# Kernel tuning notes

Measured on AMD Instinct MI355X. Metric: run time of the kernel, lower is better.

## Reference

```python
import jax, jax.numpy as jnp
import numpy as np
from jax import lax

D = 256; NH = 8; LYR = 2; G = 64; K = G * G; T = 4; EC = 32
B = 4; N = 512; CITY = 256; DFF = 4 * D

def _conv(x, w):
    return lax.conv_general_dilated(x, w, (1, 1), 'SAME', dimension_numbers=('NCHW', 'OIHW', 'NCHW'))

def _ln(x, w, b):
    m = x.mean(-1, keepdims=True)
    v = ((x - m) ** 2).mean(-1, keepdims=True)
    return (x - m) / jnp.sqrt(v + 1e-5) * w + b

def _mlp(x, w1, b1, w2, b2):
    return jax.nn.gelu(x @ w1 + b1) @ w2 + b2

def setup_inputs():
    key = jax.random.key(0)
    ks = iter(jax.random.split(key, 64))
    def nrm(shape, s=0.02):
        return jax.random.normal(next(ks), shape, jnp.float32) * s
    return {
        'meas_xy': jax.random.uniform(next(ks), (B, N, 2), jnp.float32),
        'meas_v': jax.random.normal(next(ks), (B, N), jnp.float32),
        'bs_xy': jax.random.uniform(next(ks), (B, 1, 2), jnp.float32),
        'task_id': jax.random.randint(next(ks), (B,), 0, T),
        'city': jax.random.uniform(next(ks), (B, CITY, CITY), jnp.float32),
        'mp_w1': nrm((3, D)), 'mp_b1': jnp.zeros((D,)), 'mp_w2': nrm((D, D)), 'mp_b2': jnp.zeros((D,)),
        'bp_w1': nrm((2, D)), 'bp_b1': jnp.zeros((D,)), 'bp_w2': nrm((D, D)), 'bp_b2': jnp.zeros((D,)),
        'env_w1': nrm((EC, 1, 3, 3)), 'env_b1': jnp.zeros((EC,)),
        'env_w2': nrm((EC, EC, 3, 3)), 'env_b2': jnp.zeros((EC,)),
        'env_w3': nrm((D, EC, 1, 1)), 'env_b3': jnp.zeros((D,)),
        'task_emb': nrm((T, D)), 'tp_w': nrm((D, D)), 'tp_b': jnp.zeros((D,)),
        'grid_pos': nrm((K, D)),
        'blk_dens_w': nrm((LYR, D)), 'blk_dens_b': jnp.zeros((LYR, D)),
        'blk_ln1_w': jnp.ones((LYR, D)), 'blk_ln1_b': jnp.zeros((LYR, D)),
        'blk_wq': nrm((LYR, D, D)), 'blk_bq': jnp.zeros((LYR, D)),
        'blk_wk': nrm((LYR, D, D)), 'blk_bk': jnp.zeros((LYR, D)),
        'blk_wv': nrm((LYR, D, D)), 'blk_bv': jnp.zeros((LYR, D)),
        'blk_wo': nrm((LYR, D, D)), 'blk_bo': jnp.zeros((LYR, D)),
        'blk_ln2_w': jnp.ones((LYR, D)), 'blk_ln2_b': jnp.zeros((LYR, D)),
        'blk_ff_w1': nrm((LYR, D, DFF)), 'blk_ff_b1': jnp.zeros((LYR, DFF)),
        'blk_ff_w2': nrm((LYR, DFF, D)), 'blk_ff_b2': jnp.zeros((LYR, D)),
        'tfp_w': nrm((T, D, D)), 'tfp_b': jnp.zeros((T, D)),
        'head_w': nrm((D, 1)), 'head_b': jnp.zeros((1,)),
    }

def reference(meas_xy, meas_v, bs_xy, task_id, city, mp_w1, mp_b1, mp_w2, mp_b2, bp_w1, bp_b1, bp_w2, bp_b2, env_w1, env_b1, env_w2, env_b2, env_w3, env_b3, task_emb, tp_w, tp_b, grid_pos, blk_dens_w, blk_dens_b, blk_ln1_w, blk_ln1_b, blk_wq, blk_bq, blk_wk, blk_bk, blk_wv, blk_bv, blk_wo, blk_bo, blk_ln2_w, blk_ln2_b, blk_ff_w1, blk_ff_b1, blk_ff_w2, blk_ff_b2, tfp_w, tfp_b, head_w, head_b):
    b = meas_xy.shape[0]
    dh = D // NH
    # normalized grid cell centers, [K,2] in (x,y) order
    c = (jnp.arange(G, dtype=jnp.float32) + 0.5) / G
    gy, gx = jnp.meshgrid(c, c, indexing='ij')
    grid_xy = jnp.stack([gx, gy], -1).reshape(K, 2)
    meas_tok = _mlp(jnp.concatenate([meas_xy, meas_v[..., None]], -1), mp_w1, mp_b1, mp_w2, mp_b2)
    bs_tok = _mlp(bs_xy, bp_w1, bp_b1, bp_w2, bp_b2)
    src = jnp.concatenate([meas_tok, bs_tok], 1)       # [B,Ns,D]
    src_xy = jnp.concatenate([meas_xy, bs_xy], 1)      # [B,Ns,2]
    # distance bias: [B,K,Ns]
    attn_bias = -jnp.linalg.norm(grid_xy[None, :, None, :] - src_xy[:, None, :, :], axis=-1)
    # gaussian measurement density: [B,K]
    diff = grid_xy[None, :, None, :] - meas_xy[:, None, :, :]
    dist2 = (diff * diff).sum(-1)
    sigma = 0.08
    density = jnp.exp(-dist2 / (2.0 * sigma * sigma)).mean(-1)
    # env branch: nearest-resize city to GxG, small CNN
    idx = jnp.floor(jnp.arange(G) * (city.shape[1] / G)).astype(jnp.int32)
    city_grid = city[:, idx][:, :, idx][:, None]       # [B,1,G,G]
    h = jax.nn.gelu(_conv(city_grid, env_w1) + env_b1[None, :, None, None])
    h = jax.nn.gelu(_conv(h, env_w2) + env_b2[None, :, None, None])
    env_map = _conv(h, env_w3) + env_b3[None, :, None, None]
    env_grid = env_map.transpose(0, 2, 3, 1).reshape(b, K, D)
    task_vec = (task_emb[task_id] @ tp_w + tp_b)[:, None, :]
    grid = grid_pos[None] + task_vec + env_grid
    inv_sqrt = jnp.float32(1.0 / np.sqrt(dh))
    for l in range(LYR):
        # density modulation injected into the grid latent
        g = grid + density[..., None] * blk_dens_w[l] + blk_dens_b[l]
        hn = _ln(g, blk_ln1_w[l], blk_ln1_b[l])
        q = (hn @ blk_wq[l] + blk_bq[l]).reshape(b, K, NH, dh)
        kk = (src @ blk_wk[l] + blk_bk[l]).reshape(b, -1, NH, dh)
        vv = (src @ blk_wv[l] + blk_bv[l]).reshape(b, -1, NH, dh)
        scores = jnp.einsum('bkhd,bnhd->bhkn', q, kk) * inv_sqrt + attn_bias[:, None]
        a = jax.nn.softmax(scores, -1)
        o = jnp.einsum('bhkn,bnhd->bkhd', a, vv).reshape(b, K, D) @ blk_wo[l] + blk_bo[l]
        g = g + o
        g = g + _mlp(_ln(g, blk_ln2_w[l], blk_ln2_b[l]), blk_ff_w1[l], blk_ff_b1[l], blk_ff_w2[l], blk_ff_b2[l])
        grid = g
    # per-sample task projection from the weight bank
    tf = jax.nn.gelu(jnp.einsum('bkd,bdh->bkh', grid, tfp_w[task_id]) + tfp_b[task_id][:, None, :])
    logits = (tf @ head_w + head_b)[..., 0].reshape(b, G, G)
    return logits
```

## Files before the change

### kernel.cpp

```cpp
#include <hip/hip_runtime.h>
#include <hip/hip_bf16.h>
#include <math.h>

#define D 256
#define NH 8
#define DH 32
#define LYR 2
#define G 64
#define KK 4096
#define T 4
#define EC 32
#define B 4
#define N 512
#define CITY 256
#define DFF 1024
#define NS 513
#define NSP 544
#define MSRC 2052
#define MSRCP 2176
#define ISQ 0.17677669529663687f
#define LOG2E 1.4426950408889634f

typedef short bf16x8 __attribute__((ext_vector_type(8)));
typedef float f32x4 __attribute__((ext_vector_type(4)));

__device__ __forceinline__ float gelu_f(float x) {
    const float c = 0.7978845608028654f;
    float x3 = x * x * x;
    return 0.5f * x * (1.f + tanhf(c * (x + 0.044715f * x3)));
}

__device__ __forceinline__ unsigned short f2bf(float f) {
    unsigned int u = __float_as_uint(f);
    unsigned int r = (u + 0x7FFFu + ((u >> 16) & 1u)) >> 16;
    return (unsigned short)r;
}

__device__ __forceinline__ float bf2f(unsigned short u) {
    return __uint_as_float((unsigned)u << 16);
}

__device__ __forceinline__ unsigned cvtpk(float a, float b) {
    unsigned r;
    asm("v_cvt_pk_bf16_f32 %0, %1, %2" : "=v"(r) : "v"(a), "v"(b));
    return r;
}

__device__ __forceinline__ void gl2lds16(const unsigned short* g, unsigned short* l) {
    __builtin_amdgcn_global_load_lds(
        (const __attribute__((address_space(1))) unsigned int*)g,
        (__attribute__((address_space(3))) unsigned int*)l, 16, 0, 0);
}

__global__ __launch_bounds__(256) void pre1_k(
    const float* __restrict__ wq, const float* __restrict__ wk,
    const float* __restrict__ wv, const float* __restrict__ wo,
    const float* __restrict__ ff1, const float* __restrict__ ff2,
    const float* __restrict__ tfp,
    const float* __restrict__ bk, const float* __restrict__ bv,
    unsigned short* __restrict__ wqT, unsigned short* __restrict__ kvT,
    unsigned short* __restrict__ woT, unsigned short* __restrict__ ff1T,
    unsigned short* __restrict__ ff2T, unsigned short* __restrict__ tfpT,
    float* __restrict__ kvbias,
    const float* __restrict__ meas_xy, const float* __restrict__ meas_v,
    const float* __restrict__ bs_xy,
    const float* __restrict__ mp_w1, const float* __restrict__ mp_b1,
    const float* __restrict__ mp_w2, const float* __restrict__ mp_b2,
    const float* __restrict__ bp_w1, const float* __restrict__ bp_b1,
    const float* __restrict__ bp_w2, const float* __restrict__ bp_b2,
    unsigned short* __restrict__ srcbf, float* __restrict__ src_xy,
    float* __restrict__ dens,
    const float* __restrict__ city, const float* __restrict__ env_w1,
    const float* __restrict__ env_b1, float* __restrict__ h1,
    const float* __restrict__ task_emb, const int* __restrict__ task_id,
    const float* __restrict__ tp_w, const float* __restrict__ tp_b,
    float* __restrict__ tvec,
    unsigned short* __restrict__ khd, unsigned short* __restrict__ vch)
{
    __shared__ float sh[1088];
    int bx = blockIdx.x;
    int tid = threadIdx.x;
    if (bx < 1792) {
        const float* src; unsigned short* dst;
        int Kd, Nn, nmat, rowOff = 0, t; size_t matStride;
        if (bx < 512) {
            int job = bx >> 7; t = bx & 127;
            Kd = 256; Nn = 256; nmat = 2;
            if (job == 0)      { src = wq; dst = wqT; matStride = 65536; }
            else if (job == 1) { src = wk; dst = kvT; matStride = 131072; }
            else if (job == 2) { src = wv; dst = kvT; matStride = 131072; rowOff = 256; }
            else               { src = wo; dst = woT; matStride = 65536; }
            if ((t & 63) == 0 && job == 1) kvbias[(t >> 6) * 512 + tid] = bk[(t >> 6) * 256 + tid];
            if ((t & 63) == 0 && job == 2) kvbias[(t >> 6) * 512 + 256 + tid] = bv[(t >> 6) * 256 + tid];
        } else if (bx < 1024) { t = bx - 512;  src = ff1; dst = ff1T; Kd = 256;  Nn = 1024; nmat = 2; matStride = 262144; }
        else if (bx < 1536)   { t = bx - 1024; src = ff2; dst = ff2T; Kd = 1024; Nn = 256;  nmat = 2; matStride = 262144; }
        else                  { t = bx - 1536; src = tfp; dst = tfpT; Kd = 256;  Nn = 256;  nmat = 4; matStride = 65536; }
        int tn = Nn / 32, perMat = tn * (Kd / 32);
        int mat = t / perMat;
        int rem = t - mat * perMat;
        int nb = (rem % tn) * 32, kb = (rem / tn) * 32;
        const float* s = src + (size_t)mat * Kd * Nn;
        unsigned short* d = dst + (size_t)mat * matStride;
        float (*tb)[33] = (float (*)[33])sh;
        int tx = tid & 31, ty = tid >> 5;
        #pragma unroll
        for (int i = 0; i < 4; i++)
            tb[ty + i * 8][tx] = s[(size_t)(kb + ty + i * 8) * Nn + nb + tx];
        __syncthreads();
        #pragma unroll
        for (int i = 0; i < 4; i++)
            d[(size_t)(rowOff + nb + ty + i * 8) * Kd + kb + tx] = f2bf(tb[tx][ty + i * 8]);
    } else if (bx < 3968) {
        int id = bx - 1792;
        int dd = tid;
        if (id >= B * N + B) {
            srcbf[(size_t)id * D + dd] = 0;
            return;
        }
        float* hid = sh;
        int row;
        const float *w1, *b1, *w2, *b2;
        float x0, x1, x2 = 0.f;
        int nin;
        if (id < B * N) {
            int b = id >> 9, n = id & 511;
            x0 = meas_xy[(b * N + n) * 2 + 0];
            x1 = meas_xy[(b * N + n) * 2 + 1];
            x2 = meas_v[b * N + n];
            w1 = mp_w1; b1 = mp_b1; w2 = mp_w2; b2 = mp_b2; nin = 3;
            row = b * NS + n;
        } else {
            int b = id - B * N;
            x0 = bs_xy[b * 2 + 0];
            x1 = bs_xy[b * 2 + 1];
            w1 = bp_w1; b1 = bp_b1; w2 = bp_w2; b2 = bp_b2; nin = 2;
            row = b * NS + N;
        }
        float h = x0 * w1[dd] + x1 * w1[D + dd] + b1[dd];
        if (nin == 3) h += x2 * w1[2 * D + dd];
        hid[dd] = gelu_f(h);
        __syncthreads();
        float o = b2[dd];
        for (int j = 0; j < D; j++) o += hid[j] * w2[j * D + dd];
        srcbf[(size_t)row * D + dd] = f2bf(o);
        if (dd == 0) { src_xy[row * 2 + 0] = x0; src_xy[row * 2 + 1] = x1; }
    } else if (bx < 4032) {
        int blk = bx - 3968;
        int b = blk >> 4, kc = blk & 15;
        int k = kc * 256 + tid;
        float* mx = sh; float* my = sh + 512;
        for (int i = tid; i < N; i += 256) {
            mx[i] = meas_xy[(b * N + i) * 2 + 0];
            my[i] = meas_xy[(b * N + i) * 2 + 1];
        }
        __syncthreads();
        float gx = ((k & 63) + 0.5f) / 64.f;
        float gy = ((k >> 6) + 0.5f) / 64.f;
        float s = 0.f;
        for (int n = 0; n < N; n++) {
            float dx = gx - mx[n], dy = gy - my[n];
            s += __expf(-(dx * dx + dy * dy) * 78.125f);
        }
        dens[b * KK + k] = s * (1.f / (float)N);
    } else if (bx < 6080) {
        int i = (bx - 4032) * 256 + tid;
        int x = i & 63, y = (i >> 6) & 63, c = (i >> 12) & 31, b = i >> 17;
        float s = env_b1[c];
        for (int ky = 0; ky < 3; ky++) {
            int yy = y + ky - 1;
            if (yy < 0 || yy >= G) continue;
            for (int kx = 0; kx < 3; kx++) {
                int xx = x + kx - 1;
                if (xx < 0 || xx >= G) continue;
                s += city[(b * CITY + yy * 4) * CITY + xx * 4] * env_w1[c * 9 + ky * 3 + kx];
            }
        }
        h1[i] = gelu_f(s);
    } else if (bx < 6084) {
        int b = bx - 6080;
        float* e = sh;
        e[tid] = task_emb[task_id[b] * D + tid];
        __syncthreads();
        float s = tp_b[tid];
        for (int j = 0; j < D; j++) s += e[j] * tp_w[j * D + tid];
        tvec[b * D + tid] = s;
    } else {
        int bh = bx - 6084;
        unsigned short* kp = khd + ((size_t)bh * 544 + 513) * 32;
        for (int i = tid; i < 992; i += 256) kp[i] = 0;
        unsigned short* vp = vch + ((size_t)bh * 17 + 16) * 1024;
        for (int i = tid; i < 1024; i += 256) vp[i] = 0;
    }
}

__global__ __launch_bounds__(256) void conv2_k(
    const float* __restrict__ h1, const float* __restrict__ w,
    const float* __restrict__ bias, float* __restrict__ h2) {
    int blk = blockIdx.x;
    int yt = blk & 15, cg = (blk >> 4) & 7, b = blk >> 7;
    int x = threadIdx.x & 63, y = yt * 4 + (threadIdx.x >> 6);
    int c0 = cg * 4;
    float flag[9];
    int off[9];
    #pragma unroll
    for (int ky = 0; ky < 3; ky++) {
        int yy = y + ky - 1;
        bool vy = (yy >= 0 && yy < G);
        int yc = min(max(yy, 0), G - 1);
        #pragma unroll
        for (int kx = 0; kx < 3; kx++) {
            int xx = x + kx - 1;
            bool vx = (xx >= 0 && xx < G);
            int xc = min(max(xx, 0), G - 1);
            flag[ky * 3 + kx] = (vy && vx) ? 1.f : 0.f;
            off[ky * 3 + kx] = yc * G + xc;
        }
    }
    const float* hp = h1 + ((size_t)(b * EC) << 12);
    float acc[4] = {bias[c0], bias[c0 + 1], bias[c0 + 2], bias[c0 + 3]};
    float v[9], nv[9];
    #pragma unroll
    for (int t = 0; t < 9; t++) v[t] = hp[off[t]] * flag[t];
    for (int ci = 0; ci < EC; ci++) {
        if (ci < EC - 1) {
            const float* hn = hp + ((size_t)(ci + 1) << 12);
            #pragma unroll
            for (int t = 0; t < 9; t++) nv[t] = hn[off[t]] * flag[t];
        }
        #pragma unroll
        for (int cc = 0; cc < 4; cc++) {
            const float* wp = w + ((size_t)(c0 + cc) * EC + ci) * 9;
            #pragma unroll
            for (int t = 0; t < 9; t++) acc[cc] += v[t] * wp[t];
        }
        #pragma unroll
        for (int t = 0; t < 9; t++) v[t] = nv[t];
    }
    size_t obase = (((size_t)(b * EC + c0)) << 12) + y * G + x;
    #pragma unroll
    for (int cc = 0; cc < 4; cc++)
        h2[obase + ((size_t)cc << 12)] = gelu_f(acc[cc]);
}

__global__ __launch_bounds__(256) void pre2_k(
    const float* __restrict__ h2, const float* __restrict__ w3,
    const float* __restrict__ b3, const float* __restrict__ grid_pos,
    const float* __restrict__ tvec, float* __restrict__ grid,
    const float* __restrict__ sxy, unsigned short* __restrict__ nd,
    float* __restrict__ out, const float* __restrict__ head_b)
{
    __shared__ float sh[1088];
    int bx = blockIdx.x;
    int tid = threadIdx.x;
    if (bx < 2048) {
        int b = bx >> 9, k0 = (bx & 511) * 8;
        float (*h2s)[8] = (float (*)[8])sh;
        h2s[tid >> 3][tid & 7] = h2[(((size_t)b * EC + (tid >> 3)) << 12) + k0 + (tid & 7)];
        float w3r[32];
        #pragma unroll
        for (int c4 = 0; c4 < 8; c4++) {
            float4 w4 = *(const float4*)(w3 + tid * 32 + c4 * 4);
            w3r[c4 * 4 + 0] = w4.x; w3r[c4 * 4 + 1] = w4.y;
            w3r[c4 * 4 + 2] = w4.z; w3r[c4 * 4 + 3] = w4.w;
        }
        float base = b3[tid] + tvec[b * D + tid];
        __syncthreads();
        #pragma unroll
        for (int j = 0; j < 8; j++) {
            float s = base + grid_pos[(size_t)(k0 + j) * D + tid];
            #pragma unroll
            for (int ci = 0; ci < 32; ci++) s += h2s[ci][j] * w3r[ci];
            grid[((size_t)b * KK + k0 + j) * D + tid] = s;
        }
    } else if (bx < 2304) {
        int q = bx - 2048;
        int b = q >> 6, qt = q & 63;
        float* sxs = sh; float* sys = sh + 544;
        for (int i = tid; i < 544; i += 256) {
            float x = 0.f, y = 0.f;
            if (i < NS) { x = sxy[(b * NS + i) * 2]; y = sxy[(b * NS + i) * 2 + 1]; }
            sxs[i] = x; sys[i] = y;
        }
        __syncthreads();
        unsigned short* base = nd + (size_t)q * 34816;
        for (int c = 0; c < 17; c++) {
            #pragma unroll
            for (int it = 0; it < 2; it++) {
                int lin = it * 256 + tid;
                int w16 = lin & 63, q4 = (lin >> 6) & 3, half = lin >> 8;
                int qidx = qt * 64 + w16;
                float gx = ((qidx & 63) + 0.5f) * (1.f / 64.f);
                float gy = ((qidx >> 6) + 0.5f) * (1.f / 64.f);
                unsigned short vs[4];
                #pragma unroll
                for (int r = 0; r < 4; r++) {
                    int tok = c * 32 + half * 16 + q4 * 4 + r;
                    float val;
                    if (tok < NS) {
                        float dx = gx - sxs[tok], dy = gy - sys[tok];
                        val = -sqrtf(dx * dx + dy * dy);
                    } else val = -1e4f;
                    vs[r] = f2bf(val * LOG2E);
                }
                ushort4 o; o.x = vs[0]; o.y = vs[1]; o.z = vs[2]; o.w = vs[3];
                *(ushort4*)(base + (size_t)c * 2048 + lin * 4) = o;
            }
        }
    } else {
        out[(bx - 2304) * 256 + tid] = head_b[0];
    }
}

template <int DENS>
__global__ __launch_bounds__(256) void dens_ln_k(
    float* __restrict__ grid, const float* __restrict__ dens,
    const float* __restrict__ dw, const float* __restrict__ db,
    const float* __restrict__ lw, const float* __restrict__ lb,
    unsigned short* __restrict__ y) {
    int row = blockIdx.x * 4 + (threadIdx.x >> 6);
    int lane = threadIdx.x & 63;
    float* gp = grid + (size_t)row * D + lane * 4;
    float4 v = *(float4*)gp;
    if (DENS) {
        float de = dens[row];
        float4 w4 = *(const float4*)(dw + lane * 4);
        float4 b4 = *(const float4*)(db + lane * 4);
        v.x += de * w4.x + b4.x; v.y += de * w4.y + b4.y;
        v.z += de * w4.z + b4.z; v.w += de * w4.w + b4.w;
        *(float4*)gp = v;
    }
    float s = v.x + v.y + v.z + v.w;
    #pragma unroll
    for (int o = 32; o > 0; o >>= 1) s += __shfl_xor(s, o);
    float mean = s * (1.f / D);
    float cx = v.x - mean, cy = v.y - mean, cz = v.z - mean, cw = v.w - mean;
    float q = cx * cx + cy * cy + cz * cz + cw * cw;
    #pragma unroll
    for (int o = 32; o > 0; o >>= 1) q += __shfl_xor(q, o);
    float inv = rsqrtf(q * (1.f / D) + 1e-5f);
    float4 lwv = *(const float4*)(lw + lane * 4);
    float4 lbv = *(const float4*)(lb + lane * 4);
    ushort4 o4;
    o4.x = f2bf(cx * inv * lwv.x + lbv.x);
    o4.y = f2bf(cy * inv * lwv.y + lbv.y);
    o4.z = f2bf(cz * inv * lwv.z + lbv.z);
    o4.w = f2bf(cw * inv * lwv.w + lbv.w);
    *(ushort4*)(y + (size_t)row * D + lane * 4) = o4;
}

template <int GELU, int ACCUM, int OBF, int TFPH, int STBF, int KVT = 0>
__device__ __forceinline__ void gemm_core(
    const unsigned short* __restrict__ A, const unsigned short* __restrict__ Wt,
    const float* __restrict__ bias, void* __restrict__ Cv,
    int M, int K, int Nn, int bn, int bm,
    const float* __restrict__ hw, unsigned short* __restrict__ Xb, float scale,
    unsigned short* As, unsigned short* Bs) {
    int tid = threadIdx.x;
    int wave = tid >> 6, lane = tid & 63;
    int q4 = lane >> 4, lr = lane & 15;
    int wn = wave * 16;
    int srow = tid >> 2, sk8 = (tid & 3) * 8;
    const unsigned short* Ap  = A  + (size_t)(bm + srow) * K + sk8;
    const unsigned short* Bp0 = Wt + (size_t)(bn + srow) * K + sk8;
    unsigned short* AsD = As + tid * 8;
    unsigned short* BsD = Bs + tid * 8;
    f32x4 acc[4] = {};

    gl2lds16(Ap,       AsD);
    gl2lds16(Ap + 32,  AsD + 2048);
    gl2lds16(Bp0,      BsD);
    gl2lds16(Bp0 + 32, BsD + 2048);

    int nk = K >> 6;
    for (int ki = 0; ki < nk; ki++) {
        __syncthreads();
        if (ki + 1 < nk) {
            int k0 = (ki + 1) << 6;
            int nb = ((ki + 1) & 1) * 4096;
            gl2lds16(Ap + k0,       AsD + nb);
            gl2lds16(Ap + k0 + 32,  AsD + nb + 2048);
            gl2lds16(Bp0 + k0,      BsD + nb);
            gl2lds16(Bp0 + k0 + 32, BsD + nb + 2048);
        }
        int cb = (ki & 1) * 4096;
        #pragma unroll
        for (int ks = 0; ks < 2; ks++) {
            bf16x8 af[4], bf;
            #pragma unroll
            for (int i = 0; i < 4; i++)
                af[i] = *(const bf16x8*)&As[cb + ks * 2048 + (i * 16 + lr) * 32 + q4 * 8];
            bf = *(const bf16x8*)&Bs[cb + ks * 2048 + (wn + lr) * 32 + q4 * 8];
            #pragma unroll
            for (int i = 0; i < 4; i++)
                acc[i] = __builtin_amdgcn_mfma_f32_16x16x32_bf16(af[i], bf, acc[i], 0, 0, 0);
        }
    }

    if (KVT) {
        int gc = bn + wn + lr;
        float bv = bias[gc];
        bool isV = gc >= 256;
        #pragma unroll
        for (int i = 0; i < 4; i++) {
            #pragma unroll
            for (int r = 0; r < 4; r++) {
                int gr = bm + i * 16 + q4 * 4 + r;
                if (gr < MSRC) {
                    float v = acc[i][r] + bv;
                    int bb = gr / NS;
                    int tok = gr - bb * NS;
                    if (!isV) {
                        int h = gc >> 5, dh = gc & 31;
                        ((unsigned short*)Cv)[(((size_t)(bb * 8 + h) * 544) + tok) * 32 + dh] = f2bf(v);
                    } else {
                        int gcv = gc - 256;
                        int h = gcv >> 5, dh = gcv & 31;
                        int c = tok >> 5, t32 = tok & 31;
                        Xb[((((size_t)(bb * 8 + h) * 17 + c) * 32 + dh)) * 32 + t32] = f2bf(v);
                    }
                }
            }
        }
        return;
    }

    if (TFPH) {
        int gc = bn + wn + lr;
        float bv = bias[gc];
        float hv = hw[gc];
        #pragma unroll
        for (int i = 0; i < 4; i++) {
            #pragma unroll
            for (int r = 0; r < 4; r++) {
                float s = gelu_f(acc[i][r] + bv) * hv;
                s += __shfl_xor(s, 1); s += __shfl_xor(s, 2);
                s += __shfl_xor(s, 4); s += __shfl_xor(s, 8);
                if (lr == 0)
                    atomicAdd((float*)Cv + (bm + i * 16 + q4 * 4 + r), s);
            }
        }
        return;
    }

    int gc = bn + wn + lr;
    float bv = bias[gc];
    #pragma unroll
    for (int i = 0; i < 4; i++) {
        #pragma unroll
        for (int r = 0; r < 4; r++) {
            int gr = bm + i * 16 + q4 * 4 + r;
            if (gr < M) {
                float v = (acc[i][r] + bv) * scale;
                if (GELU) v = gelu_f(v);
                size_t idx = (size_t)gr * Nn + gc;
                if (OBF) {
                    ((unsigned short*)Cv)[idx] = f2bf(v);
                } else if (ACCUM) {
                    float nv = ((float*)Cv)[idx] + v;
                    ((float*)Cv)[idx] = nv;
                    if (STBF) Xb[idx] = f2bf(nv);
                } else {
                    ((float*)Cv)[idx] = v;
                }
            }
        }
    }
}

template <int GELU, int ACCUM, int OBF, int TFPH, int STBF>
__global__ __launch_bounds__(256) void gemm_k(
    const unsigned short* __restrict__ A, const unsigned short* __restrict__ Wt0,
    const float* __restrict__ bias0, void* __restrict__ Cv,
    int M, int K, int Nn, const int* __restrict__ task_id,
    const float* __restrict__ hw, unsigned short* __restrict__ Xb) {
    __shared__ unsigned short As[8192];
    __shared__ unsigned short Bs[8192];
    const unsigned short* Wt = Wt0;
    const float* bias = bias0;
    int bm = blockIdx.y * 64;
    if (TFPH) { int t = task_id[bm >> 12]; Wt += (size_t)t * D * D; bias += t * D; }
    gemm_core<GELU, ACCUM, OBF, TFPH, STBF>(A, Wt, bias, Cv, M, K, Nn,
                                            blockIdx.x * 64, bm, hw, Xb, 1.f, As, Bs);
}

__global__ __launch_bounds__(256) void qkv_k(
    const unsigned short* __restrict__ xbf, const unsigned short* __restrict__ wqT,
    const float* __restrict__ bq, unsigned short* __restrict__ qbf,
    const unsigned short* __restrict__ srcbf, const unsigned short* __restrict__ kvT,
    const float* __restrict__ kvb, unsigned short* __restrict__ khd,
    unsigned short* __restrict__ vch) {
    __shared__ unsigned short As[8192];
    __shared__ unsigned short Bs[8192];
    if (blockIdx.x < 4) {
        gemm_core<0, 0, 1, 0, 0, 0>(xbf, wqT, bq, qbf, B * KK, D, D,
                                    blockIdx.x * 64, blockIdx.y * 64, nullptr, nullptr,
                                    ISQ * LOG2E, As, Bs);
    } else {
        if (blockIdx.y >= MSRCP / 64) return;
        gemm_core<0, 0, 1, 0, 0, 1>(srcbf, kvT, kvb, khd, MSRC, D, 512,
                                    (blockIdx.x - 4) * 64, blockIdx.y * 64, nullptr, vch, 1.f, As, Bs);
    }
}

__global__ __launch_bounds__(256) void attn_mfma(
    const unsigned short* __restrict__ qb,
    const unsigned short* __restrict__ khd,
    const unsigned short* __restrict__ vch,
    const unsigned short* __restrict__ ndL,
    unsigned short* __restrict__ out)
{
    int bid = blockIdx.x;
    int qt = bid & 63, h = (bid >> 6) & 7, b = bid >> 9;
    int tid = threadIdx.x, wave = tid >> 6, lane = tid & 63;
    int q4 = lane >> 4, lr = lane & 15;

    int kbase = qt * 64 + wave * 16;
    size_t qrow = (size_t)(b * KK + kbase + lr);
    bf16x8 qf = *(const bf16x8*)(qb + qrow * D + h * DH + q4 * 8);
    const unsigned short* kp0 = khd + ((size_t)(b * 8 + h) * 544) * 32 + lr * 32 + q4 * 8;
    const unsigned short* vb0 = vch + ((size_t)(b * 8 + h) * 17) * 1024 + lr * 32 + q4 * 8;
    const unsigned short* ndp = ndL + ((size_t)(b * 64 + qt)) * 34816 + q4 * 256 + (wave * 16 + lr) * 4;

    float ll0 = 0.f, ll1 = 0.f;
    f32x4 o0 = {0.f, 0.f, 0.f, 0.f}, o1 = {0.f, 0.f, 0.f, 0.f};
    int sA = ((lane >> 4) & 1) * 32 + lr;
    int sB = sA + 16;
    bool hi = (lane & 32) != 0;

    bf16x8 kf0 = *(const bf16x8*)kp0;
    bf16x8 kf1 = *(const bf16x8*)(kp0 + 512);
    bf16x8 vt0 = *(const bf16x8*)vb0;
    bf16x8 vt1 = *(const bf16x8*)(vb0 + 512);
    ushort4 n0v = *(const ushort4*)ndp;
    ushort4 n1v = *(const ushort4*)(ndp + 1024);

    for (int c = 0; c < 17; c++) {
        bf16x8 ck0 = kf0, ck1 = kf1, cv0 = vt0, cv1 = vt1;
        ushort4 cn0 = n0v, cn1 = n1v;
        if (c < 16) {
            size_t co = (size_t)(c + 1) * 1024;
            kf0 = *(const bf16x8*)(kp0 + co);
            kf1 = *(const bf16x8*)(kp0 + co + 512);
            vt0 = *(const bf16x8*)(vb0 + co);
            vt1 = *(const bf16x8*)(vb0 + co + 512);
            n0v = *(const ushort4*)(ndp + (size_t)(c + 1) * 2048);
            n1v = *(const ushort4*)(ndp + (size_t)(c + 1) * 2048 + 1024);
        }
        f32x4 s0 = {0.f, 0.f, 0.f, 0.f}, s1 = {0.f, 0.f, 0.f, 0.f};
        s0 = __builtin_amdgcn_mfma_f32_16x16x32_bf16(ck0, qf, s0, 0, 0, 0);
        s1 = __builtin_amdgcn_mfma_f32_16x16x32_bf16(ck1, qf, s1, 0, 0, 0);
        float p0[4], p1[4];
        p0[0] = __builtin_amdgcn_exp2f(s0[0] + bf2f(cn0.x));
        p0[1] = __builtin_amdgcn_exp2f(s0[1] + bf2f(cn0.y));
        p0[2] = __builtin_amdgcn_exp2f(s0[2] + bf2f(cn0.z));
        p0[3] = __builtin_amdgcn_exp2f(s0[3] + bf2f(cn0.w));
        p1[0] = __builtin_amdgcn_exp2f(s1[0] + bf2f(cn1.x));
        p1[1] = __builtin_amdgcn_exp2f(s1[1] + bf2f(cn1.y));
        p1[2] = __builtin_amdgcn_exp2f(s1[2] + bf2f(cn1.z));
        p1[3] = __builtin_amdgcn_exp2f(s1[3] + bf2f(cn1.w));
        ll0 += (p0[0] + p0[1]) + (p0[2] + p0[3]);
        ll1 += (p1[0] + p1[1]) + (p1[2] + p1[3]);
        unsigned pk0 = cvtpk(p0[0], p0[1]);
        unsigned pk1 = cvtpk(p0[2], p0[3]);
        unsigned pk2 = cvtpk(p1[0], p1[1]);
        unsigned pk3 = cvtpk(p1[2], p1[3]);
        unsigned a0 = (unsigned)__shfl((int)pk0, sA), c0 = (unsigned)__shfl((int)pk2, sA);
        unsigned a1 = (unsigned)__shfl((int)pk1, sA), c1 = (unsigned)__shfl((int)pk3, sA);
        unsigned a2 = (unsigned)__shfl((int)pk0, sB), c2 = (unsigned)__shfl((int)pk2, sB);
        unsigned a3 = (unsigned)__shfl((int)pk1, sB), c3 = (unsigned)__shfl((int)pk3, sB);
        union { unsigned u[4]; bf16x8 v; } pu;
        pu.u[0] = hi ? c0 : a0;
        pu.u[1] = hi ? c1 : a1;
        pu.u[2] = hi ? c2 : a2;
        pu.u[3] = hi ? c3 : a3;
        o0 = __builtin_amdgcn_mfma_f32_16x16x32_bf16(cv0, pu.v, o0, 0, 0, 0);
        o1 = __builtin_amdgcn_mfma_f32_16x16x32_bf16(cv1, pu.v, o1, 0, 0, 0);
    }

    float ll = ll0 + ll1;
    ll += __shfl_xor(ll, 16);
    ll += __shfl_xor(ll, 32);
    float inv = 1.f / ll;
    unsigned w0 = cvtpk(o0[0] * inv, o0[1] * inv);
    unsigned w1 = cvtpk(o0[2] * inv, o0[3] * inv);
    unsigned w2 = cvtpk(o1[0] * inv, o1[1] * inv);
    unsigned w3 = cvtpk(o1[2] * inv, o1[3] * inv);
    uint2 st0; st0.x = w0; st0.y = w1;
    uint2 st1; st1.x = w2; st1.y = w3;
    *(uint2*)(out + qrow * D + h * DH + q4 * 4) = st0;
    *(uint2*)(out + qrow * D + h * DH + 16 + q4 * 4) = st1;
}

extern "C" void kernel_launch(void* const* d_in, const int* in_sizes, int n_in,
                              void* d_out, int out_size, void* d_ws, size_t ws_size,
                              hipStream_t stream) {
    const float* meas_xy = (const float*)d_in[0];
    const float* meas_v  = (const float*)d_in[1];
    const float* bs_xy   = (const float*)d_in[2];
    const int*   task_id = (const int*)d_in[3];
    const float* city    = (const float*)d_in[4];
    const float* mp_w1 = (const float*)d_in[5];  const float* mp_b1 = (const float*)d_in[6];
    const float* mp_w2 = (const float*)d_in[7];  const float* mp_b2 = (const float*)d_in[8];
    const float* bp_w1 = (const float*)d_in[9];  const float* bp_b1 = (const float*)d_in[10];
    const float* bp_w2 = (const float*)d_in[11]; const float* bp_b2 = (const float*)d_in[12];
    const float* env_w1 = (const float*)d_in[13]; const float* env_b1 = (const float*)d_in[14];
    const float* env_w2 = (const float*)d_in[15]; const float* env_b2 = (const float*)d_in[16];
    const float* env_w3 = (const float*)d_in[17]; const float* env_b3 = (const float*)d_in[18];
    const float* task_emb = (const float*)d_in[19];
    const float* tp_w = (const float*)d_in[20]; const float* tp_b = (const float*)d_in[21];
    const float* grid_pos = (const float*)d_in[22];
    const float* dens_w = (const float*)d_in[23]; const float* dens_b = (const float*)d_in[24];
    const float* ln1_w = (const float*)d_in[25]; const float* ln1_b = (const float*)d_in[26];
    const float* wq = (const float*)d_in[27]; const float* bq = (const float*)d_in[28];
    const float* wk = (const float*)d_in[29]; const float* bk = (const float*)d_in[30];
    const float* wv = (const float*)d_in[31]; const float* bv = (const float*)d_in[32];
    const float* wo = (const float*)d_in[33]; const float* bo = (const float*)d_in[34];
    const float* ln2_w = (const float*)d_in[35]; const float* ln2_b = (const float*)d_in[36];
    const float* ff_w1 = (const float*)d_in[37]; const float* ff_b1 = (const float*)d_in[38];
    const float* ff_w2 = (const float*)d_in[39]; const float* ff_b2 = (const float*)d_in[40];
    const float* tfp_w = (const float*)d_in[41]; const float* tfp_b = (const float*)d_in[42];
    const float* head_w = (const float*)d_in[43]; const float* head_b = (const float*)d_in[44];
    float* out = (float*)d_out;

    float* ws = (float*)d_ws;
    size_t off = 0;
    float* src_xy = ws + off; off += (size_t)B * NS * 2 + 128;
    float* dens   = ws + off; off += (size_t)B * KK;
    float* tvec   = ws + off; off += (size_t)B * D;
    float* h1     = ws + off; off += (size_t)B * EC * KK;
    float* grid   = ws + off; off += (size_t)B * KK * D;
    unsigned short* srcbf = (unsigned short*)(ws + off); off += (size_t)MSRCP * D / 2;
    unsigned short* khd   = (unsigned short*)(ws + off); off += (size_t)B * 8 * 544 * 32 / 2;
    unsigned short* vch   = (unsigned short*)(ws + off); off += (size_t)B * 8 * 17 * 1024 / 2;
    float* qreg   = ws + off; off += (size_t)B * KK * D / 2;
    unsigned short* qbf = (unsigned short*)qreg;
    float* h2     = qreg;
    unsigned short* xbf    = (unsigned short*)(ws + off); off += (size_t)B * KK * D / 2;
    unsigned short* attnbf = (unsigned short*)(ws + off); off += (size_t)B * KK * D / 2;
    unsigned short* ndbf   = (unsigned short*)(ws + off); off += (size_t)B * 64 * 34816 / 2;
    unsigned short* hidbf  = (unsigned short*)(ws + off); off += (size_t)B * KK * DFF / 2;
    unsigned short* wqT  = (unsigned short*)(ws + off); off += (size_t)LYR * D * D / 2;
    unsigned short* kvT  = (unsigned short*)(ws + off); off += (size_t)LYR * 512 * D / 2;
    unsigned short* woT  = (unsigned short*)(ws + off); off += (size_t)LYR * D * D / 2;
    unsigned short* ff1T = (unsigned short*)(ws + off); off += (size_t)LYR * D * DFF / 2;
    unsigned short* ff2T = (unsigned short*)(ws + off); off += (size_t)LYR * DFF * D / 2;
    unsigned short* tfpT = (unsigned short*)(ws + off); off += (size_t)T * D * D / 2;
    float* kvbias = ws + off; off += (size_t)LYR * 512;
    (void)ws_size; (void)n_in; (void)in_sizes; (void)out_size;

    const int M = B * KK;

    pre1_k<<<6116, 256, 0, stream>>>(
        wq, wk, wv, wo, ff_w1, ff_w2, tfp_w, bk, bv,
        wqT, kvT, woT, ff1T, ff2T, tfpT, kvbias,
        meas_xy, meas_v, bs_xy, mp_w1, mp_b1, mp_w2, mp_b2,
        bp_w1, bp_b1, bp_w2, bp_b2, srcbf, src_xy,
        dens, city, env_w1, env_b1, h1,
        task_emb, task_id, tp_w, tp_b, tvec, khd, vch);
    conv2_k<<<512, 256, 0, stream>>>(h1, env_w2, env_b2, h2);
    pre2_k<<<2368, 256, 0, stream>>>(h2, env_w3, env_b3, grid_pos, tvec, grid,
                                     src_xy, ndbf, out, head_b);

    for (int l = 0; l < LYR; l++) {
        dens_ln_k<1><<<M / 4, 256, 0, stream>>>(grid, dens, dens_w + l * D, dens_b + l * D,
                                                ln1_w + l * D, ln1_b + l * D, xbf);
        qkv_k<<<dim3(12, 256), 256, 0, stream>>>(
            xbf, wqT + (size_t)l * D * D, bq + l * D, qbf,
            srcbf, kvT + (size_t)l * 512 * D, kvbias + l * 512, khd, vch);
        attn_mfma<<<B * NH * 64, 256, 0, stream>>>(qbf, khd, vch, ndbf, attnbf);
        gemm_k<0, 1, 0, 0, 0><<<dim3(4, 256), 256, 0, stream>>>(
            attnbf, woT + (size_t)l * D * D, bo + l * D, grid, M, D, D, nullptr, nullptr, nullptr);
        dens_ln_k<0><<<M / 4, 256, 0, stream>>>(grid, nullptr, nullptr, nullptr,
                                                ln2_w + l * D, ln2_b + l * D, xbf);
        gemm_k<1, 0, 1, 0, 0><<<dim3(16, 256), 256, 0, stream>>>(
            xbf, ff1T + (size_t)l * D * DFF, ff_b1 + l * DFF, hidbf, M, D, DFF,
            nullptr, nullptr, nullptr);
        if (l == 0) {
            gemm_k<0, 1, 0, 0, 0><<<dim3(4, 256), 256, 0, stream>>>(
                hidbf, ff2T + (size_t)l * DFF * D, ff_b2 + l * D, grid, M, DFF, D,
                nullptr, nullptr, nullptr);
        } else {
            gemm_k<0, 1, 0, 0, 1><<<dim3(4, 256), 256, 0, stream>>>(
                hidbf, ff2T + (size_t)l * DFF * D, ff_b2 + l * D, grid, M, DFF, D,
                nullptr, nullptr, xbf);
        }
    }
    gemm_k<1, 0, 0, 1, 0><<<dim3(4, 256), 256, 0, stream>>>(
        xbf, tfpT, tfp_b, out, M, D, D, task_id, head_w, nullptr);
}
```

Measured before the change: 575.3 us.

## Enlarge GEMM M-tile to 128 rows and use exp2-based GELU

The shared GEMM core now computes a 128x64 output tile per block instead of 64x64, doubling the A staging buffer and reusing each B fragment across eight MFMAs. All GEMM launches halve their grid in y to match. The intent is to cut B-operand LDS reads and global reloads per output, at the cost of more accumulator registers and LDS per block, which can lower occupancy. GELU is also rewritten as x*sigmoid-style exp2/rcp instead of tanhf, trading some precision for fewer instructions.

```diff
diff --git a/kernel.cpp b/kernel.cpp
--- a/kernel.cpp
+++ b/kernel.cpp
@@ -25,9 +25,11 @@
 typedef float f32x4 __attribute__((ext_vector_type(4)));
 
 __device__ __forceinline__ float gelu_f(float x) {
-    const float c = 0.7978845608028654f;
-    float x3 = x * x * x;
-    return 0.5f * x * (1.f + tanhf(c * (x + 0.044715f * x3)));
+    const float c2 = 2.f * LOG2E * 0.7978845608028654f;
+    float u = x + 0.044715f * x * x * x;
+    float a = fminf(c2 * u, 80.f);
+    float t = __builtin_amdgcn_exp2f(a);
+    return x * t * __builtin_amdgcn_rcpf(t + 1.f);
 }
 
 __device__ __forceinline__ unsigned short f2bf(float f) {
@@ -360,39 +362,44 @@
     int q4 = lane >> 4, lr = lane & 15;
     int wn = wave * 16;
     int srow = tid >> 2, sk8 = (tid & 3) * 8;
-    const unsigned short* Ap  = A  + (size_t)(bm + srow) * K + sk8;
-    const unsigned short* Bp0 = Wt + (size_t)(bn + srow) * K + sk8;
+    const unsigned short* Ap0 = A  + (size_t)(bm + srow) * K + sk8;
+    const unsigned short* Ap1 = A  + (size_t)(bm + 64 + srow) * K + sk8;
+    const unsigned short* Bp  = Wt + (size_t)(bn + srow) * K + sk8;
     unsigned short* AsD = As + tid * 8;
     unsigned short* BsD = Bs + tid * 8;
-    f32x4 acc[4] = {};
-
-    gl2lds16(Ap,       AsD);
-    gl2lds16(Ap + 32,  AsD + 2048);
-    gl2lds16(Bp0,      BsD);
-    gl2lds16(Bp0 + 32, BsD + 2048);
+    f32x4 acc[8] = {};
+
+    gl2lds16(Ap0,      AsD);
+    gl2lds16(Ap1,      AsD + 2048);
+    gl2lds16(Ap0 + 32, AsD + 4096);
+    gl2lds16(Ap1 + 32, AsD + 4096 + 2048);
+    gl2lds16(Bp,       BsD);
+    gl2lds16(Bp + 32,  BsD + 2048);
 
     int nk = K >> 6;
     for (int ki = 0; ki < nk; ki++) {
         __syncthreads();
         if (ki + 1 < nk) {
             int k0 = (ki + 1) << 6;
-            int nb = ((ki + 1) & 1) * 4096;
-            gl2lds16(Ap + k0,       AsD + nb);
-            gl2lds16(Ap + k0 + 32,  AsD + nb + 2048);
-            gl2lds16(Bp0 + k0,      BsD + nb);
-            gl2lds16(Bp0 + k0 + 32, BsD + nb + 2048);
-        }
-        int cb = (ki & 1) * 4096;
+            int nbA = ((ki + 1) & 1) * 8192;
+            int nbB = ((ki + 1) & 1) * 4096;
+            gl2lds16(Ap0 + k0,      AsD + nbA);
+            gl2lds16(Ap1 + k0,      AsD + nbA + 2048);
+            gl2lds16(Ap0 + k0 + 32, AsD + nbA + 4096);
+            gl2lds16(Ap1 + k0 + 32, AsD + nbA + 4096 + 2048);
+            gl2lds16(Bp + k0,       BsD + nbB);
+            gl2lds16(Bp + k0 + 32,  BsD + nbB + 2048);
+        }
+        int cbA = (ki & 1) * 8192;
+        int cbB = (ki & 1) * 4096;
         #pragma unroll
         for (int ks = 0; ks < 2; ks++) {
-            bf16x8 af[4], bf;
+            bf16x8 bf = *(const bf16x8*)&Bs[cbB + ks * 2048 + (wn + lr) * 32 + q4 * 8];
             #pragma unroll
-            for (int i = 0; i < 4; i++)
-                af[i] = *(const bf16x8*)&As[cb + ks * 2048 + (i * 16 + lr) * 32 + q4 * 8];
-            bf = *(const bf16x8*)&Bs[cb + ks * 2048 + (wn + lr) * 32 + q4 * 8];
-            #pragma unroll
-            for (int i = 0; i < 4; i++)
-                acc[i] = __builtin_amdgcn_mfma_f32_16x16x32_bf16(af[i], bf, acc[i], 0, 0, 0);
+            for (int i = 0; i < 8; i++) {
+                bf16x8 af = *(const bf16x8*)&As[cbA + ks * 4096 + (i * 16 + lr) * 32 + q4 * 8];
+                acc[i] = __builtin_amdgcn_mfma_f32_16x16x32_bf16(af, bf, acc[i], 0, 0, 0);
+            }
         }
     }
 
@@ -401,7 +408,7 @@
         float bv = bias[gc];
         bool isV = gc >= 256;
         #pragma unroll
-        for (int i = 0; i < 4; i++) {
+        for (int i = 0; i < 8; i++) {
             #pragma unroll
             for (int r = 0; r < 4; r++) {
                 int gr = bm + i * 16 + q4 * 4 + r;
@@ -429,7 +436,7 @@
         float bv = bias[gc];
         float hv = hw[gc];
         #pragma unroll
-        for (int i = 0; i < 4; i++) {
+        for (int i = 0; i < 8; i++) {
             #pragma unroll
             for (int r = 0; r < 4; r++) {
                 float s = gelu_f(acc[i][r] + bv) * hv;
@@ -445,7 +452,7 @@
     int gc = bn + wn + lr;
     float bv = bias[gc];
     #pragma unroll
-    for (int i = 0; i < 4; i++) {
+    for (int i = 0; i < 8; i++) {
         #pragma unroll
         for (int r = 0; r < 4; r++) {
             int gr = bm + i * 16 + q4 * 4 + r;
@@ -473,11 +480,11 @@
     const float* __restrict__ bias0, void* __restrict__ Cv,
     int M, int K, int Nn, const int* __restrict__ task_id,
     const float* __restrict__ hw, unsigned short* __restrict__ Xb) {
-    __shared__ unsigned short As[8192];
+    __shared__ unsigned short As[16384];
     __shared__ unsigned short Bs[8192];
     const unsigned short* Wt = Wt0;
     const float* bias = bias0;
-    int bm = blockIdx.y * 64;
+    int bm = blockIdx.y * 128;
     if (TFPH) { int t = task_id[bm >> 12]; Wt += (size_t)t * D * D; bias += t * D; }
     gemm_core<GELU, ACCUM, OBF, TFPH, STBF>(A, Wt, bias, Cv, M, K, Nn,
                                             blockIdx.x * 64, bm, hw, Xb, 1.f, As, Bs);
@@ -489,16 +496,16 @@
     const unsigned short* __restrict__ srcbf, const unsigned short* __restrict__ kvT,
     const float* __restrict__ kvb, unsigned short* __restrict__ khd,
     unsigned short* __restrict__ vch) {
-    __shared__ unsigned short As[8192];
+    __shared__ unsigned short As[16384];
     __shared__ unsigned short Bs[8192];
     if (blockIdx.x < 4) {
         gemm_core<0, 0, 1, 0, 0, 0>(xbf, wqT, bq, qbf, B * KK, D, D,
-                                    blockIdx.x * 64, blockIdx.y * 64, nullptr, nullptr,
+                                    blockIdx.x * 64, blockIdx.y * 128, nullptr, nullptr,
                                     ISQ * LOG2E, As, Bs);
     } else {
-        if (blockIdx.y >= MSRCP / 64) return;
+        if (blockIdx.y >= MSRCP / 128) return;
         gemm_core<0, 0, 1, 0, 0, 1>(srcbf, kvT, kvb, khd, MSRC, D, 512,
-                                    (blockIdx.x - 4) * 64, blockIdx.y * 64, nullptr, vch, 1.f, As, Bs);
+                                    (blockIdx.x - 4) * 64, blockIdx.y * 128, nullptr, vch, 1.f, As, Bs);
     }
 }
 
@@ -664,27 +671,27 @@
     for (int l = 0; l < LYR; l++) {
         dens_ln_k<1><<<M / 4, 256, 0, stream>>>(grid, dens, dens_w + l * D, dens_b + l * D,
                                                 ln1_w + l * D, ln1_b + l * D, xbf);
-        qkv_k<<<dim3(12, 256), 256, 0, stream>>>(
+        qkv_k<<<dim3(12, 128), 256, 0, stream>>>(
             xbf, wqT + (size_t)l * D * D, bq + l * D, qbf,
             srcbf, kvT + (size_t)l * 512 * D, kvbias + l * 512, khd, vch);
         attn_mfma<<<B * NH * 64, 256, 0, stream>>>(qbf, khd, vch, ndbf, attnbf);
-        gemm_k<0, 1, 0, 0, 0><<<dim3(4, 256), 256, 0, stream>>>(
+        gemm_k<0, 1, 0, 0, 0><<<dim3(4, 128), 256, 0, stream>>>(
             attnbf, woT + (size_t)l * D * D, bo + l * D, grid, M, D, D, nullptr, nullptr, nullptr);
         dens_ln_k<0><<<M / 4, 256, 0, stream>>>(grid, nullptr, nullptr, nullptr,
                                                 ln2_w + l * D, ln2_b + l * D, xbf);
-        gemm_k<1, 0, 1, 0, 0><<<dim3(16, 256), 256, 0, stream>>>(
+        gemm_k<1, 0, 1, 0, 0><<<dim3(16, 128), 256, 0, stream>>>(
             xbf, ff1T + (size_t)l * D * DFF, ff_b1 + l * DFF, hidbf, M, D, DFF,
             nullptr, nullptr, nullptr);
         if (l == 0) {
-            gemm_k<0, 1, 0, 0, 0><<<dim3(4, 256), 256, 0, stream>>>(
+            gemm_k<0, 1, 0, 0, 0><<<dim3(4, 128), 256, 0, stream>>>(
                 hidbf, ff2T + (size_t)l * DFF * D, ff_b2 + l * D, grid, M, DFF, D,
                 nullptr, nullptr, nullptr);
         } else {
-            gemm_k<0, 1, 0, 0, 1><<<dim3(4, 256), 256, 0, stream>>>(
+            gemm_k<0, 1, 0, 0, 1><<<dim3(4, 128), 256, 0, stream>>>(
                 hidbf, ff2T + (size_t)l * DFF * D, ff_b2 + l * D, grid, M, DFF, D,
                 nullptr, nullptr, xbf);
         }
     }
-    gemm_k<1, 0, 0, 1, 0><<<dim3(4, 256), 256, 0, stream>>>(
+    gemm_k<1, 0, 0, 1, 0><<<dim3(4, 128), 256, 0, stream>>>(
         xbf, tfpT, tfp_b, out, M, D, D, task_id, head_w, nullptr);
 }
```

Result: no change. 586.6 us (+2.0%).
